# Kernel optimization log

Measured on AMD Instinct MI355X. Metric: run time of the kernel, lower is better.

The kernel has to match this reference:

```python
import jax, jax.numpy as jnp
import numpy as np
import math

N, IN_DIM, Z, H, OUT, K = 16384, 64, 128, 1, 3, 16


def setup_inputs() -> dict:
    key = jax.random.key(0)
    ks = jax.random.split(key, 16)

    def lin(k, din, dout):
        kw, kb = jax.random.split(k)
        W = jax.random.normal(kw, (din, dout), jnp.float32) / math.sqrt(din)
        b = jax.random.normal(kb, (dout,), jnp.float32) * 0.01
        return W, b

    x = jax.random.normal(ks[0], (N, IN_DIM), jnp.float32)
    t = jnp.zeros((1,), jnp.float32)
    # layer dims: (in, heads*out) per TransformerConv
    dims = [(IN_DIM, Z * H), (Z * H, (Z // H) * H), (Z * H, (OUT // H) * H)]
    params = {}
    i = 1
    for li, (din, dout) in enumerate(dims, 1):
        for nm in ("q", "k", "v", "s"):
            W, b = lin(ks[i], din, dout)
            i += 1
            params[f"W{nm}{li}"] = W
            params[f"b{nm}{li}"] = b
    return {"t": t, "x": x, **params}


def knn_edge_index(coo, k):
    # kNN graph on 3-D coords (loop=False): edges neighbor(src) -> center(dst)
    n = coo.shape[0]
    sq = jnp.sum(coo * coo, axis=-1)
    d = sq[:, None] + sq[None, :] - 2.0 * (coo @ coo.T)  # [N, N] sq. distances
    d = d.at[jnp.arange(n), jnp.arange(n)].set(jnp.inf)  # exclude self-loops
    _, idx = jax.lax.top_k(-d, k)  # [N, K] nearest neighbor indices
    src = idx.reshape(-1)
    dst = jnp.repeat(jnp.arange(n), k)
    return src, dst


def tconv(x, src, dst, Wq, bq, Wk, bk, Wv, bv, Ws, bs, heads):
    # PyG TransformerConv (concat=True, root_weight=True, no edge_attr)
    n = x.shape[0]
    dout = Wq.shape[1]
    c = dout // heads
    q = (x @ Wq + bq).reshape(n, heads, c)
    kk = (x @ Wk + bk).reshape(n, heads, c)
    v = (x @ Wv + bv).reshape(n, heads, c)
    alpha = jnp.sum(q[dst] * kk[src], axis=-1) / math.sqrt(c)  # [E, H]
    amax = jax.ops.segment_max(alpha, dst, num_segments=n)
    ex = jnp.exp(alpha - amax[dst])
    denom = jax.ops.segment_sum(ex, dst, num_segments=n)
    w = ex / denom[dst]  # softmax over incoming edges per node
    msg = w[:, :, None] * v[src]  # [E, H, C]
    out = jax.ops.segment_sum(msg, dst, num_segments=n).reshape(n, dout)
    return out + x @ Ws + bs  # root/skip connection


def reference(t, x,
              Wq1, bq1, Wk1, bk1, Wv1, bv1, Ws1, bs1,
              Wq2, bq2, Wk2, bk2, Wv2, bv2, Ws2, bs2,
              Wq3, bq3, Wk3, bk3, Wv3, bv3, Ws3, bs3):
    src, dst = knn_edge_index(x[:, :3], K)  # built under no_grad in original
    h = jnp.tanh(tconv(x, src, dst, Wq1, bq1, Wk1, bk1, Wv1, bv1, Ws1, bs1, H))
    h = jnp.tanh(tconv(h, src, dst, Wq2, bq2, Wk2, bk2, Wv2, bv2, Ws2, bs2, H) + h)
    drift_coo = tconv(h, src, dst, Wq3, bq3, Wk3, bk3, Wv3, bv3, Ws3, bs3, H)
    return drift_coo
```

## Files before the change

### kernel.cpp

```cpp
#include <hip/hip_runtime.h>
#include <math.h>

#define NN 16384
#define CAP 128
#define WM 64
#define KTOP 17
#define NSLAB 128
#define SH 0.0625f
#define SHI 16.0f

typedef unsigned long long u64;

__device__ __forceinline__ int mbcnt64(u64 mask) {
  return __builtin_amdgcn_mbcnt_hi(
      (unsigned)(mask >> 32),
      __builtin_amdgcn_mbcnt_lo((unsigned)mask, 0));
}

__device__ __forceinline__ unsigned fmap(float d) {
  unsigned ub = __float_as_uint(d);
  return ub ^ ((unsigned)((int)ub >> 31) | 0x80000000u);
}

__device__ __forceinline__ float unfmap(unsigned ub) {
  unsigned fb = (ub & 0x80000000u) ? (ub ^ 0x80000000u) : ~ub;
  return __uint_as_float(fb);
}

__device__ __forceinline__ unsigned short f2bf(float f) {
  unsigned u = __float_as_uint(f);
  return (unsigned short)((u + 0x7FFFu + ((u >> 16) & 1u)) >> 16);
}
__device__ __forceinline__ float bf2f(unsigned short h) {
  return __uint_as_float(((unsigned)h) << 16);
}

__device__ __forceinline__ u64 u64min(u64 a, u64 b) { return a < b ? a : b; }
__device__ __forceinline__ u64 u64max(u64 a, u64 b) { return a > b ? a : b; }

__device__ __forceinline__ int slabof(float v) {
  int c = (int)floorf((v + 4.0f) * SHI);
  return c < 0 ? 0 : (c > NSLAB - 1 ? NSLAB - 1 : c);
}

__device__ __forceinline__ void sort64(u64& r0, int lane) {
#pragma unroll
  for (int k = 2; k <= 64; k <<= 1) {
#pragma unroll
    for (int jj = k >> 1; jj >= 1; jj >>= 1) {
      const bool up = (lane & jj) == 0;
      const bool asc = (lane & k) == 0;
      u64 o = __shfl_xor(r0, jj);
      r0 = (up == asc) ? u64min(r0, o) : u64max(r0, o);
    }
  }
}

__device__ __forceinline__ void radix_shrink(u64* buf, int& cnt, float& cq,
                                             int lane) {
  const u64 k0 = (lane < cnt) ? buf[lane] : ~0ull;
  const u64 k1 = (lane + 64 < cnt) ? buf[lane + 64] : ~0ull;
  const unsigned d0 = (unsigned)(k0 >> 32);
  const unsigned d1 = (unsigned)(k1 >> 32);
  unsigned p = 0u;
#pragma unroll
  for (int b = 31; b >= 0; --b) {
    const unsigned c = p | (1u << b);
    const u64 b0 = __ballot(d0 < c);
    const u64 b1 = __ballot(d1 < c);
    const int n = __popcll(b0) + __popcll(b1);
    if (n < KTOP) p = c;
  }
  const bool v0 = d0 <= p;
  const bool v1 = d1 <= p;
  const u64 m0 = __ballot(v0);
  const u64 m1 = __ballot(v1);
  const int base = __popcll(m0);
  if (v0) buf[mbcnt64(m0)] = k0;
  if (v1) buf[base + mbcnt64(m1)] = k1;
  cnt = base + __popcll(m1);
  cq = -unfmap(p);
}

__global__ __launch_bounds__(256) void pack_slabs(const float* __restrict__ x,
                                                  float4* __restrict__ tmp4,
                                                  int* __restrict__ sid,
                                                  unsigned* __restrict__ hist) {
  const int i = blockIdx.x * 256 + threadIdx.x;
  const float a = x[i * 64 + 0];
  const float b = x[i * 64 + 1];
  const float c = x[i * 64 + 2];
  tmp4[i] = make_float4(a, b, c, -0.5f * (a * a + b * b + c * c));
  const int s = slabof(c);
  sid[i] = s;
  atomicAdd(&hist[s], 1u);
}

__global__ __launch_bounds__(128) void prefix_slabs(
    const unsigned* __restrict__ hist, unsigned* __restrict__ slabstart,
    unsigned* __restrict__ slabfill) {
  __shared__ unsigned ls[NSLAB];
  const int t = threadIdx.x;
  const unsigned h = hist[t];
  ls[t] = h;
  __syncthreads();
  for (int off = 1; off < NSLAB; off <<= 1) {
    const unsigned v = (t >= off) ? ls[t - off] : 0u;
    __syncthreads();
    ls[t] += v;
    __syncthreads();
  }
  const unsigned ex = ls[t] - h;
  slabstart[t] = ex;
  slabfill[t] = ex;
  if (t == NSLAB - 1) slabstart[NSLAB] = ls[t];
}

__global__ __launch_bounds__(256) void scatter_slabs(
    const float4* __restrict__ tmp4, const int* __restrict__ sid,
    unsigned* __restrict__ slabfill, float4* __restrict__ sorted4,
    int* __restrict__ sidx) {
  const int i = blockIdx.x * 256 + threadIdx.x;
  const unsigned pos = atomicAdd(&slabfill[sid[i]], 1u);
  sorted4[pos] = tmp4[i];
  sidx[pos] = i;
}

__global__ __launch_bounds__(256) void knn_z(
    const float4* __restrict__ sorted4, const int* __restrict__ sidx,
    const unsigned* __restrict__ slabstart, int* __restrict__ src) {
  __shared__ u64 bufs_[4][2][CAP];
  const int lane = threadIdx.x & 63;
  const int wid = threadIdx.x >> 6;
  u64* buf0 = bufs_[wid][0];
  u64* buf1 = bufs_[wid][1];
  const int qpos = blockIdx.x * 8 + wid * 2;
  const float4 m0 = sorted4[qpos];
  const float4 m1 = sorted4[qpos + 1];
  const float qx0 = m0.x, qy0 = m0.y, qz0 = m0.z, q20 = -2.0f * m0.w;
  const float qx1 = m1.x, qy1 = m1.y, qz1 = m1.z, q21 = -2.0f * m1.w;
  float cq0 = -INFINITY, cq1 = -INFINITY;
  int cnt0 = 0, cnt1 = 0;

  auto scan_range = [&](int s, int e) {
    if (s >= e) return;
    int o = s;
    float4 p = sorted4[(s + lane) < e ? (s + lane) : s];
    while (o < e) {
      const int on = o + 64;
      float4 pn;
      if (on < e) {
        const int jn = on + lane;
        pn = sorted4[jn < e ? jn : s];
      }
      const int j = o + lane;
      const bool in = j < e;
      const float L0 = fmaf(qx0, p.x, fmaf(qy0, p.y, fmaf(qz0, p.z, p.w)));
      const float L1 = fmaf(qx1, p.x, fmaf(qy1, p.y, fmaf(qz1, p.z, p.w)));
      const bool p0 = in && (L0 >= cq0);
      const bool p1 = in && (L1 >= cq1);
      const u64 mk0 = __ballot(p0);
      const u64 mk1 = __ballot(p1);
      if (mk0 | mk1) {
        if (mk0) {
          if (p0)
            buf0[cnt0 + mbcnt64(mk0)] =
                ((u64)fmap(-L0) << 32) | (unsigned)sidx[j];
          cnt0 += __popcll(mk0);
          if (cnt0 >= WM) radix_shrink(buf0, cnt0, cq0, lane);
        }
        if (mk1) {
          if (p1)
            buf1[cnt1 + mbcnt64(mk1)] =
                ((u64)fmap(-L1) << 32) | (unsigned)sidx[j];
          cnt1 += __popcll(mk1);
          if (cnt1 >= WM) radix_shrink(buf1, cnt1, cq1, lane);
        }
      }
      o = on;
      p = pn;
    }
  };

  int slo = slabof(qz0) - 2;
  if (slo < 0) slo = 0;
  int shi = slabof(qz1) + 2;
  if (shi > NSLAB - 1) shi = NSLAB - 1;
  scan_range((int)slabstart[slo], (int)slabstart[shi + 1]);

  const float zmin = fminf(qz0, qz1), zmax = fmaxf(qz0, qz1);
  while (true) {
    if (cnt0 >= KTOP) radix_shrink(buf0, cnt0, cq0, lane);
    if (cnt1 >= KTOP) radix_shrink(buf1, cnt1, cq1, lane);
    int rlo, rhi;
    if (cnt0 >= KTOP && cnt1 >= KTOP) {
      const float d0 = fmaxf(fmaf(-2.0f, cq0, q20), 0.0f);
      const float d1 = fmaxf(fmaf(-2.0f, cq1, q21), 0.0f);
      const float rneed = sqrtf(fmaxf(d0, d1) * 1.00002f + 1e-4f);
      rlo = (int)floorf((zmin - rneed + 4.0f) * SHI);
      rhi = (int)floorf((zmax + rneed + 4.0f) * SHI);
      if (rlo < 0) rlo = 0;
      if (rhi > NSLAB - 1) rhi = NSLAB - 1;
      if (rlo > slo) rlo = slo;
      if (rhi < shi) rhi = shi;
    } else {
      rlo = slo - 4;
      if (rlo < 0) rlo = 0;
      rhi = shi + 4;
      if (rhi > NSLAB - 1) rhi = NSLAB - 1;
    }
    bool ext = false;
    if (rlo < slo) {
      scan_range((int)slabstart[rlo], (int)slabstart[slo]);
      slo = rlo;
      ext = true;
    }
    if (rhi > shi) {
      scan_range((int)slabstart[shi + 1], (int)slabstart[rhi + 1]);
      shi = rhi;
      ext = true;
    }
    if (!ext) break;
  }

#pragma unroll 1
  for (int q = 0; q < 2; ++q) {
    u64* buf = q == 0 ? buf0 : buf1;
    int cnt = q == 0 ? cnt0 : cnt1;
    float cqd = q == 0 ? cq0 : cq1;
    if (cnt > 64) radix_shrink(buf, cnt, cqd, lane);
    const int qorig = sidx[qpos + q];
    u64 r0 = (lane < cnt) ? buf[lane] : ~0ull;
    sort64(r0, lane);
    const int idx = (int)(r0 & 0xFFFFFFFFull);
    const u64 selfm = __ballot((lane < KTOP) && (idx == qorig));
    const int sp = selfm ? (__ffsll((long long)selfm) - 1) : 99;
    const int outrank = lane - (lane > sp ? 1 : 0);
    if (lane < KTOP && lane != sp && outrank < 16)
      src[qorig * 16 + outrank] = idx;
  }
}

template <int KD>
__global__ __launch_bounds__(256) void gemm_qkvs(
    const float* __restrict__ X, const float* __restrict__ W0,
    const float* __restrict__ W1, const float* __restrict__ W2,
    const float* __restrict__ W3, const float* __restrict__ B0,
    const float* __restrict__ B1, const float* __restrict__ B2,
    const float* __restrict__ B3, float* __restrict__ qs,
    unsigned short* __restrict__ kvh) {
  __shared__ float As[64][68];
  __shared__ float Bs[64][64];
  const int brow = blockIdx.x * 64;
  const int by = blockIdx.y;
  const int wi = by >> 1;
  const float* W = wi == 0 ? W0 : wi == 1 ? W1 : wi == 2 ? W2 : W3;
  const float* bias = wi == 0 ? B0 : wi == 1 ? B1 : wi == 2 ? B2 : B3;
  const int cbase = (by & 1) * 64;
  const int tx = threadIdx.x & 15;
  const int ty = threadIdx.x >> 4;

  float acc[4][4] = {};
  for (int k0 = 0; k0 < KD; k0 += 64) {
    __syncthreads();
#pragma unroll
    for (int i = 0; i < 4; ++i) {
      const int flat = threadIdx.x * 4 + i * 1024;
      const int r = flat >> 6, kk = flat & 63;
      const float4 v = *(const float4*)&X[(brow + r) * KD + k0 + kk];
      As[kk + 0][r] = v.x;
      As[kk + 1][r] = v.y;
      As[kk + 2][r] = v.z;
      As[kk + 3][r] = v.w;
    }
#pragma unroll
    for (int i = 0; i < 4; ++i) {
      const int flat = threadIdx.x * 4 + i * 1024;
      const int kk = flat >> 6, c = flat & 63;
      *(float4*)&Bs[kk][c] = *(const float4*)&W[(k0 + kk) * 128 + cbase + c];
    }
    __syncthreads();
#pragma unroll 8
    for (int k = 0; k < 64; ++k) {
      const float4 a = *(const float4*)&As[k][ty * 4];
      const float4 b = *(const float4*)&Bs[k][tx * 4];
      const float av[4] = {a.x, a.y, a.z, a.w};
      const float bv[4] = {b.x, b.y, b.z, b.w};
#pragma unroll
      for (int i = 0; i < 4; ++i)
#pragma unroll
        for (int jj = 0; jj < 4; ++jj)
          acc[i][jj] = fmaf(av[i], bv[jj], acc[i][jj]);
    }
  }
  const float4 bi = *(const float4*)&bias[cbase + tx * 4];
  const int col = cbase + tx * 4;
#pragma unroll
  for (int i = 0; i < 4; ++i) {
    const int row = brow + ty * 4 + i;
    float4 o;
    o.x = acc[i][0] + bi.x;
    o.y = acc[i][1] + bi.y;
    o.z = acc[i][2] + bi.z;
    o.w = acc[i][3] + bi.w;
    if (wi == 0) {
      *(float4*)&qs[row * 256 + col] = o;
    } else if (wi == 3) {
      *(float4*)&qs[row * 256 + 128 + col] = o;
    } else {
      ushort4 h;
      h.x = f2bf(o.x);
      h.y = f2bf(o.y);
      h.z = f2bf(o.z);
      h.w = f2bf(o.w);
      *(ushort4*)&kvh[row * 256 + (wi == 1 ? col : 128 + col)] = h;
    }
  }
}

__global__ __launch_bounds__(256) void attn_c128(
    const float* __restrict__ qs, const unsigned short* __restrict__ kvh,
    const int* __restrict__ src, const float* __restrict__ res,
    float* __restrict__ hout, int do_res) {
  const int g = threadIdx.x >> 5;
  const int node = blockIdx.x * 8 + g;
  const int c = threadIdx.x & 31;
  const float4 q4 = ((const float4*)(qs + node * 256))[c];

  int nb[16];
#pragma unroll
  for (int r = 0; r < 16; ++r) nb[r] = src[node * 16 + r];

  float p[16];
#pragma unroll
  for (int r = 0; r < 16; ++r) {
    const ushort4 k4 = ((const ushort4*)(kvh + nb[r] * 256))[c];
    p[r] = q4.x * bf2f(k4.x) + q4.y * bf2f(k4.y) + q4.z * bf2f(k4.z) +
           q4.w * bf2f(k4.w);
  }
#pragma unroll
  for (int o = 16; o; o >>= 1) {
#pragma unroll
    for (int r = 0; r < 16; ++r) p[r] += __shfl_xor(p[r], o);
  }

  float m = p[0];
#pragma unroll
  for (int r = 1; r < 16; ++r) m = fmaxf(m, p[r]);
  float w[16];
  float den = 0.0f;
#pragma unroll
  for (int r = 0; r < 16; ++r) {
    w[r] = __expf((p[r] - m) * 0.088388347648318447f);
    den += w[r];
  }
  const float inv = 1.0f / den;
  float o0 = 0.0f, o1 = 0.0f, o2 = 0.0f, o3 = 0.0f;
#pragma unroll
  for (int r = 0; r < 16; ++r) {
    const ushort4 v4 = ((const ushort4*)(kvh + nb[r] * 256 + 128))[c];
    const float ww = w[r] * inv;
    o0 = fmaf(ww, bf2f(v4.x), o0);
    o1 = fmaf(ww, bf2f(v4.y), o1);
    o2 = fmaf(ww, bf2f(v4.z), o2);
    o3 = fmaf(ww, bf2f(v4.w), o3);
  }
  const float4 s4 = ((const float4*)(qs + node * 256 + 128))[c];
  float r0 = o0 + s4.x, r1 = o1 + s4.y, r2 = o2 + s4.z, r3 = o3 + s4.w;
  if (do_res) {
    const float4 h4 = ((const float4*)(res + node * 128))[c];
    r0 += h4.x;
    r1 += h4.y;
    r2 += h4.z;
    r3 += h4.w;
  }
  ((float4*)(hout + node * 128))[c] =
      make_float4(tanhf(r0), tanhf(r1), tanhf(r2), tanhf(r3));
}

__global__ __launch_bounds__(256) void gemm_qkvs3(
    const float* __restrict__ H, const float* __restrict__ W0,
    const float* __restrict__ W1, const float* __restrict__ W2,
    const float* __restrict__ W3, const float* __restrict__ B0,
    const float* __restrict__ B1, const float* __restrict__ B2,
    const float* __restrict__ B3, float* __restrict__ out) {
  __shared__ float hs[64][132];
  __shared__ float wsh[128 * 12];
  __shared__ float bsh[12];
  const int brow = blockIdx.x * 64;
  if (threadIdx.x < 12) {
    const int mi = threadIdx.x / 3, c = threadIdx.x % 3;
    const float* Bsel = mi == 0 ? B0 : mi == 1 ? B1 : mi == 2 ? B2 : B3;
    bsh[threadIdx.x] = Bsel[c];
  }
  for (int t = threadIdx.x; t < 1536; t += 256) {
    const int k = t / 12, cc = t % 12;
    const int mi = cc / 3, c = cc % 3;
    const float* Wsel = mi == 0 ? W0 : mi == 1 ? W1 : mi == 2 ? W2 : W3;
    wsh[t] = Wsel[k * 3 + c];
  }
#pragma unroll
  for (int i = 0; i < 8; ++i) {
    const int flat = threadIdx.x * 4 + i * 1024;
    const int r = flat >> 7, kk = flat & 127;
    *(float4*)&hs[r][kk] = *(const float4*)&H[(brow + r) * 128 + kk];
  }
  __syncthreads();
  const int r = threadIdx.x >> 2;
  const int part = threadIdx.x & 3;
  float a0 = 0.0f, a1 = 0.0f, a2 = 0.0f;
#pragma unroll 4
  for (int k = 0; k < 128; ++k) {
    const float h = hs[r][k];
    a0 = fmaf(h, wsh[k * 12 + part * 3 + 0], a0);
    a1 = fmaf(h, wsh[k * 12 + part * 3 + 1], a1);
    a2 = fmaf(h, wsh[k * 12 + part * 3 + 2], a2);
  }
  const int row = brow + r;
  out[row * 12 + part * 3 + 0] = a0 + bsh[part * 3 + 0];
  out[row * 12 + part * 3 + 1] = a1 + bsh[part * 3 + 1];
  out[row * 12 + part * 3 + 2] = a2 + bsh[part * 3 + 2];
}

__global__ __launch_bounds__(256) void attn_c3(const float* __restrict__ q3,
                                               const int* __restrict__ src,
                                               float* __restrict__ out) {
  const int gid = blockIdx.x * 256 + threadIdx.x;
  const int node = gid >> 4, r = gid & 15;
  const int j = src[node * 16 + r];
  const float* qn = q3 + node * 12;
  const float* kj = q3 + j * 12 + 3;
  float alpha = (qn[0] * kj[0] + qn[1] * kj[1] + qn[2] * kj[2]) *
                0.57735026918962576f;
  float m = alpha;
#pragma unroll
  for (int o = 8; o; o >>= 1) m = fmaxf(m, __shfl_xor(m, o, 16));
  const float e = __expf(alpha - m);
  float den = e;
#pragma unroll
  for (int o = 8; o; o >>= 1) den += __shfl_xor(den, o, 16);
  const float wgt = e / den;
  const float* vj = q3 + j * 12 + 6;
  float o0 = wgt * vj[0], o1 = wgt * vj[1], o2 = wgt * vj[2];
#pragma unroll
  for (int o = 8; o; o >>= 1) {
    o0 += __shfl_xor(o0, o, 16);
    o1 += __shfl_xor(o1, o, 16);
    o2 += __shfl_xor(o2, o, 16);
  }
  if (r == 0) {
    const float* sn = q3 + node * 12 + 9;
    out[node * 3 + 0] = o0 + sn[0];
    out[node * 3 + 1] = o1 + sn[1];
    out[node * 3 + 2] = o2 + sn[2];
  }
}

extern "C" void kernel_launch(void* const* d_in, const int* in_sizes, int n_in,
                              void* d_out, int out_size, void* d_ws,
                              size_t ws_size, hipStream_t stream) {
  const float* x = (const float*)d_in[1];
  const float* Wq1 = (const float*)d_in[2];
  const float* bq1 = (const float*)d_in[3];
  const float* Wk1 = (const float*)d_in[4];
  const float* bk1 = (const float*)d_in[5];
  const float* Wv1 = (const float*)d_in[6];
  const float* bv1 = (const float*)d_in[7];
  const float* Ws1 = (const float*)d_in[8];
  const float* bs1 = (const float*)d_in[9];
  const float* Wq2 = (const float*)d_in[10];
  const float* bq2 = (const float*)d_in[11];
  const float* Wk2 = (const float*)d_in[12];
  const float* bk2 = (const float*)d_in[13];
  const float* Wv2 = (const float*)d_in[14];
  const float* bv2 = (const float*)d_in[15];
  const float* Ws2 = (const float*)d_in[16];
  const float* bs2 = (const float*)d_in[17];
  const float* Wq3 = (const float*)d_in[18];
  const float* bq3 = (const float*)d_in[19];
  const float* Wk3 = (const float*)d_in[20];
  const float* bk3 = (const float*)d_in[21];
  const float* Wv3 = (const float*)d_in[22];
  const float* bv3 = (const float*)d_in[23];
  const float* Ws3 = (const float*)d_in[24];
  const float* bs3 = (const float*)d_in[25];

  const size_t MB = 1024 * 1024;
  const size_t KB = 1024;
  char* ws = (char*)d_ws;
  float4* tmp4 = (float4*)(ws);
  float4* sorted4 = (float4*)(ws + 256 * KB);
  int* sid = (int*)(ws + 512 * KB);
  int* sidx = (int*)(ws + 576 * KB);
  unsigned* hist = (unsigned*)(ws + 640 * KB);
  unsigned* slabstart = (unsigned*)(ws + 644 * KB);
  unsigned* slabfill = (unsigned*)(ws + 648 * KB);

  float* qs = (float*)(ws);
  unsigned short* kvh = (unsigned short*)(ws + 16 * MB);
  float* h1 = (float*)(ws + 24 * MB);
  float* h2 = (float*)(ws + 32 * MB);
  int* src = (int*)(ws + 40 * MB);
  float* q3 = (float*)(ws + 42 * MB);
  float* out = (float*)d_out;

  hipMemsetAsync(hist, 0, NSLAB * sizeof(unsigned), stream);
  pack_slabs<<<NN / 256, 256, 0, stream>>>(x, tmp4, sid, hist);
  prefix_slabs<<<1, NSLAB, 0, stream>>>(hist, slabstart, slabfill);
  scatter_slabs<<<NN / 256, 256, 0, stream>>>(tmp4, sid, slabfill, sorted4,
                                              sidx);
  knn_z<<<NN / 8, 256, 0, stream>>>(sorted4, sidx, slabstart, src);
  gemm_qkvs<64><<<dim3(NN / 64, 8), 256, 0, stream>>>(
      x, Wq1, Wk1, Wv1, Ws1, bq1, bk1, bv1, bs1, qs, kvh);
  attn_c128<<<NN / 8, 256, 0, stream>>>(qs, kvh, src, nullptr, h1, 0);
  gemm_qkvs<128><<<dim3(NN / 64, 8), 256, 0, stream>>>(
      h1, Wq2, Wk2, Wv2, Ws2, bq2, bk2, bv2, bs2, qs, kvh);
  attn_c128<<<NN / 8, 256, 0, stream>>>(qs, kvh, src, h1, h2, 1);
  gemm_qkvs3<<<NN / 64, 256, 0, stream>>>(h2, Wq3, Wk3, Wv3, Ws3, bq3, bk3,
                                          bv3, bs3, q3);
  attn_c3<<<NN * 16 / 256, 256, 0, stream>>>(q3, src, out);
}
```

Baseline: 358.0 us.

## Seed kNN candidates from sorted neighbors and replace radix shrink with bitonic sort

Before scanning slabs, each query pair first scores the 64 nearest entries in z-sorted order and shrinks them to the top 17. This gives a finite cutoff from the start, so the first slab window can be sized from the actual needed radius instead of a fixed plus-or-minus two slabs. Those 64 entries are then masked out of later scans. The 32-step ballot radix threshold search is replaced by a 128-element bitonic sort that keeps exactly 17 entries. Risks: the sort costs more shuffles per shrink, and the first window may be wider or narrower than before.

```diff
diff --git a/kernel.cpp b/kernel.cpp
--- a/kernel.cpp
+++ b/kernel.cpp
@@ -56,30 +56,36 @@
   }
 }
 
-__device__ __forceinline__ void radix_shrink(u64* buf, int& cnt, float& cq,
-                                             int lane) {
-  const u64 k0 = (lane < cnt) ? buf[lane] : ~0ull;
-  const u64 k1 = (lane + 64 < cnt) ? buf[lane + 64] : ~0ull;
-  const unsigned d0 = (unsigned)(k0 >> 32);
-  const unsigned d1 = (unsigned)(k1 >> 32);
-  unsigned p = 0u;
-#pragma unroll
-  for (int b = 31; b >= 0; --b) {
-    const unsigned c = p | (1u << b);
-    const u64 b0 = __ballot(d0 < c);
-    const u64 b1 = __ballot(d1 < c);
-    const int n = __popcll(b0) + __popcll(b1);
-    if (n < KTOP) p = c;
-  }
-  const bool v0 = d0 <= p;
-  const bool v1 = d1 <= p;
-  const u64 m0 = __ballot(v0);
-  const u64 m1 = __ballot(v1);
-  const int base = __popcll(m0);
-  if (v0) buf[mbcnt64(m0)] = k0;
-  if (v1) buf[base + mbcnt64(m1)] = k1;
-  cnt = base + __popcll(m1);
-  cq = -unfmap(p);
+__device__ __forceinline__ void sort128(u64& r0, u64& r1, int lane) {
+#pragma unroll
+  for (int k = 2; k <= 128; k <<= 1) {
+    if (k == 128) {
+      u64 lo = u64min(r0, r1);
+      r1 = u64max(r0, r1);
+      r0 = lo;
+    }
+#pragma unroll
+    for (int jj = (k == 128 ? 32 : (k >> 1)); jj >= 1; jj >>= 1) {
+      const bool up = (lane & jj) == 0;
+      const bool asc0 = (lane & k) == 0;
+      const bool asc1 = ((lane | 64) & k) == 0;
+      u64 o0 = __shfl_xor(r0, jj);
+      u64 o1 = __shfl_xor(r1, jj);
+      r0 = (up == asc0) ? u64min(r0, o0) : u64max(r0, o0);
+      r1 = (up == asc1) ? u64min(r1, o1) : u64max(r1, o1);
+    }
+  }
+}
+
+__device__ __forceinline__ void sort_shrink(u64* buf, int& cnt, float& cq,
+                                            int lane) {
+  u64 r0 = (lane < cnt) ? buf[lane] : ~0ull;
+  u64 r1 = (lane + 64 < cnt) ? buf[lane + 64] : ~0ull;
+  sort128(r0, r1, lane);
+  const u64 k17 = __shfl(r0, KTOP - 1);
+  cq = -unfmap((unsigned)(k17 >> 32));
+  if (lane < KTOP) buf[lane] = r0;
+  cnt = KTOP;
 }
 
 __global__ __launch_bounds__(256) void pack_slabs(const float* __restrict__ x,
@@ -139,8 +145,29 @@
   const float4 m1 = sorted4[qpos + 1];
   const float qx0 = m0.x, qy0 = m0.y, qz0 = m0.z, q20 = -2.0f * m0.w;
   const float qx1 = m1.x, qy1 = m1.y, qz1 = m1.z, q21 = -2.0f * m1.w;
-  float cq0 = -INFINITY, cq1 = -INFINITY;
-  int cnt0 = 0, cnt1 = 0;
+  float cq0, cq1;
+  int cnt0, cnt1;
+
+  int pf_s = qpos - 31;
+  if (pf_s < 0) pf_s = 0;
+  int pf_e = pf_s + 64;
+  if (pf_e > NN) {
+    pf_e = NN;
+    pf_s = pf_e - 64;
+  }
+  {
+    const int j = pf_s + lane;
+    const float4 p = sorted4[j];
+    const float L0 = fmaf(qx0, p.x, fmaf(qy0, p.y, fmaf(qz0, p.z, p.w)));
+    const float L1 = fmaf(qx1, p.x, fmaf(qy1, p.y, fmaf(qz1, p.z, p.w)));
+    const unsigned oi = (unsigned)sidx[j];
+    buf0[lane] = ((u64)fmap(-L0) << 32) | oi;
+    buf1[lane] = ((u64)fmap(-L1) << 32) | oi;
+    cnt0 = 64;
+    cnt1 = 64;
+    sort_shrink(buf0, cnt0, cq0, lane);
+    sort_shrink(buf1, cnt1, cq1, lane);
+  }
 
   auto scan_range = [&](int s, int e) {
     if (s >= e) return;
@@ -154,7 +181,7 @@
         pn = sorted4[jn < e ? jn : s];
       }
       const int j = o + lane;
-      const bool in = j < e;
+      const bool in = (j < e) && (j < pf_s || j >= pf_e);
       const float L0 = fmaf(qx0, p.x, fmaf(qy0, p.y, fmaf(qz0, p.z, p.w)));
       const float L1 = fmaf(qx1, p.x, fmaf(qy1, p.y, fmaf(qz1, p.z, p.w)));
       const bool p0 = in && (L0 >= cq0);
@@ -167,14 +194,14 @@
             buf0[cnt0 + mbcnt64(mk0)] =
                 ((u64)fmap(-L0) << 32) | (unsigned)sidx[j];
           cnt0 += __popcll(mk0);
-          if (cnt0 >= WM) radix_shrink(buf0, cnt0, cq0, lane);
+          if (cnt0 >= WM) sort_shrink(buf0, cnt0, cq0, lane);
         }
         if (mk1) {
           if (p1)
             buf1[cnt1 + mbcnt64(mk1)] =
                 ((u64)fmap(-L1) << 32) | (unsigned)sidx[j];
           cnt1 += __popcll(mk1);
-          if (cnt1 >= WM) radix_shrink(buf1, cnt1, cq1, lane);
+          if (cnt1 >= WM) sort_shrink(buf1, cnt1, cq1, lane);
         }
       }
       o = on;
@@ -182,33 +209,28 @@
     }
   };
 
-  int slo = slabof(qz0) - 2;
+  const float zmin = fminf(qz0, qz1), zmax = fmaxf(qz0, qz1);
+  const float di0 = fmaxf(fmaf(-2.0f, cq0, q20), 0.0f);
+  const float di1 = fmaxf(fmaf(-2.0f, cq1, q21), 0.0f);
+  const float rn0 = sqrtf(fmaxf(di0, di1) * 1.00002f + 1e-4f);
+  int slo = (int)floorf((zmin - rn0 + 4.0f) * SHI);
+  int shi = (int)floorf((zmax + rn0 + 4.0f) * SHI);
   if (slo < 0) slo = 0;
-  int shi = slabof(qz1) + 2;
   if (shi > NSLAB - 1) shi = NSLAB - 1;
   scan_range((int)slabstart[slo], (int)slabstart[shi + 1]);
 
-  const float zmin = fminf(qz0, qz1), zmax = fmaxf(qz0, qz1);
   while (true) {
-    if (cnt0 >= KTOP) radix_shrink(buf0, cnt0, cq0, lane);
-    if (cnt1 >= KTOP) radix_shrink(buf1, cnt1, cq1, lane);
-    int rlo, rhi;
-    if (cnt0 >= KTOP && cnt1 >= KTOP) {
-      const float d0 = fmaxf(fmaf(-2.0f, cq0, q20), 0.0f);
-      const float d1 = fmaxf(fmaf(-2.0f, cq1, q21), 0.0f);
-      const float rneed = sqrtf(fmaxf(d0, d1) * 1.00002f + 1e-4f);
-      rlo = (int)floorf((zmin - rneed + 4.0f) * SHI);
-      rhi = (int)floorf((zmax + rneed + 4.0f) * SHI);
-      if (rlo < 0) rlo = 0;
-      if (rhi > NSLAB - 1) rhi = NSLAB - 1;
-      if (rlo > slo) rlo = slo;
-      if (rhi < shi) rhi = shi;
-    } else {
-      rlo = slo - 4;
-      if (rlo < 0) rlo = 0;
-      rhi = shi + 4;
-      if (rhi > NSLAB - 1) rhi = NSLAB - 1;
-    }
+    if (cnt0 > KTOP) sort_shrink(buf0, cnt0, cq0, lane);
+    if (cnt1 > KTOP) sort_shrink(buf1, cnt1, cq1, lane);
+    const float d0 = fmaxf(fmaf(-2.0f, cq0, q20), 0.0f);
+    const float d1 = fmaxf(fmaf(-2.0f, cq1, q21), 0.0f);
+    const float rn = sqrtf(fmaxf(d0, d1) * 1.00002f + 1e-4f);
+    int rlo = (int)floorf((zmin - rn + 4.0f) * SHI);
+    int rhi = (int)floorf((zmax + rn + 4.0f) * SHI);
+    if (rlo < 0) rlo = 0;
+    if (rhi > NSLAB - 1) rhi = NSLAB - 1;
+    if (rlo > slo) rlo = slo;
+    if (rhi < shi) rhi = shi;
     bool ext = false;
     if (rlo < slo) {
       scan_range((int)slabstart[rlo], (int)slabstart[slo]);
@@ -227,8 +249,6 @@
   for (int q = 0; q < 2; ++q) {
     u64* buf = q == 0 ? buf0 : buf1;
     int cnt = q == 0 ? cnt0 : cnt1;
-    float cqd = q == 0 ? cq0 : cq1;
-    if (cnt > 64) radix_shrink(buf, cnt, cqd, lane);
     const int qorig = sidx[qpos + q];
     u64 r0 = (lane < cnt) ? buf[lane] : ~0ull;
     sort64(r0, lane);
```

Result: slower. 460.2 us (+28.6%).
